# Performance work log

Measured on AMD Instinct MI355X. Metric: run time of the kernel, lower is better.

The kernel has to match this reference:

```python
import jax, jax.numpy as jnp
import numpy as np

INPUT_DIM = 128
D_MODEL = 128
BATCH = 8192
EPS = 1e-5  # torch LayerNorm default


def setup_inputs() -> dict:
    key = jax.random.key(0)
    k1, k2, k3 = jax.random.split(key, 3)
    x = jax.random.normal(k1, (BATCH, INPUT_DIM), dtype=jnp.float32)
    # Per-feature Linear(1, d_model): weight is a d_model vector per feature.
    W = jax.random.normal(k2, (INPUT_DIM, D_MODEL), dtype=jnp.float32) * (1.0 / np.sqrt(D_MODEL))
    b = jax.random.normal(k3, (INPUT_DIM, D_MODEL), dtype=jnp.float32) * 0.02
    gamma = jnp.ones((D_MODEL,), dtype=jnp.float32)
    beta = jnp.zeros((D_MODEL,), dtype=jnp.float32)
    return {"x": x, "W": W, "b": b, "gamma": gamma, "beta": beta}


def reference(x, W, b, gamma, beta):
    # Fused equivalent of the per-feature Linear loop + stack(dim=0):
    # out[f, n, d] = x[n, f] * W[f, d] + b[f, d]  -> [input_dim, batch, d_model]
    emb = x.T[:, :, None] * W[:, None, :] + b[:, None, :]
    # LayerNorm over last dim (d_model), eps=1e-5, elementwise affine.
    mean = jnp.mean(emb, axis=-1, keepdims=True)
    var = jnp.mean(jnp.square(emb - mean), axis=-1, keepdims=True)
    normed = (emb - mean) * jax.lax.rsqrt(var + EPS)
    out = normed * gamma + beta
    # Dropout is identity in eval mode.
    return out
```

## Files before the change

kernel.cpp:

```cpp
#include <hip/hip_runtime.h>

#define F_DIM   128
#define D_DIM   128
#define BATCH_N 8192
#define LN_EPS  1e-5f
#define ROWS_PER_BLOCK 64

__global__ __launch_bounds__(256) void fused_emb_ln_kernel(const float* __restrict__ x,
                                                           const float* __restrict__ W,
                                                           const float* __restrict__ b,
                                                           const float* __restrict__ gamma,
                                                           const float* __restrict__ beta,
                                                           float* __restrict__ out) {
    const int tid   = threadIdx.x;
    const int f     = blockIdx.x >> 7;
    const int nbase = (blockIdx.x & 127) * ROWS_PER_BLOCK;

    __shared__ float r1[128], r2[128], r3[128];
    __shared__ float sWg[128], sBg[128], sBe[128];

    float w = 0.f, bb = 0.f, g = 0.f, be = 0.f;
    if (tid < 128) {
        w  = W[f * D_DIM + tid];
        bb = b[f * D_DIM + tid];
        g  = gamma[tid];
        be = beta[tid];
        r1[tid] = w; r2[tid] = bb;
    }
    __syncthreads();
    for (int off = 64; off > 0; off >>= 1) {
        if (tid < off) { r1[tid] += r1[tid + off]; r2[tid] += r2[tid + off]; }
        __syncthreads();
    }
    const float inv = 1.0f / 128.0f;
    const float mw  = r1[0] * inv;
    const float mbm = r2[0] * inv;
    __syncthreads();
    if (tid < 128) {
        const float wc = w - mw;
        const float bc = bb - mbm;
        r1[tid] = wc * wc; r2[tid] = wc * bc; r3[tid] = bc * bc;
        sWg[tid] = wc * g; sBg[tid] = bc * g; sBe[tid] = be;
    }
    __syncthreads();
    for (int off = 64; off > 0; off >>= 1) {
        if (tid < off) { r1[tid] += r1[tid + off]; r2[tid] += r2[tid + off]; r3[tid] += r3[tid + off]; }
        __syncthreads();
    }
    const float A  = r1[0] * inv;
    const float B2 = 2.0f * r2[0] * inv;
    const float Cp = r3[0] * inv + LN_EPS;

    const int dv = tid & 31;
    const int r0 = tid >> 5;
    const float4* Wg4 = (const float4*)sWg;
    const float4* Bg4 = (const float4*)sBg;
    const float4* Be4 = (const float4*)sBe;
    const float4 w0 = Wg4[dv];
    const float4 b0 = Bg4[dv];
    const float4 e0 = Be4[dv];

    float4* out4 = (float4*)out;
    #pragma unroll
    for (int it = 0; it < ROWS_PER_BLOCK / 8; ++it) {
        const int n  = nbase + it * 8 + r0;
        const float xf = x[n * F_DIM + f];

        float var = fmaf(xf, fmaf(xf, A, B2), Cp);
        var = fmaxf(var, 1e-7f);
        const float rsq = rsqrtf(var);
        const float xr  = xf * rsq;

        float4 o;
        o.x = fmaf(xr, w0.x, fmaf(rsq, b0.x, e0.x));
        o.y = fmaf(xr, w0.y, fmaf(rsq, b0.y, e0.y));
        o.z = fmaf(xr, w0.z, fmaf(rsq, b0.z, e0.z));
        o.w = fmaf(xr, w0.w, fmaf(rsq, b0.w, e0.w));

        out4[(f * BATCH_N + n) * 32 + dv] = o;
    }
}

extern "C" void kernel_launch(void* const* d_in, const int* in_sizes, int n_in,
                              void* d_out, int out_size, void* d_ws, size_t ws_size,
                              hipStream_t stream) {
    const float* x     = (const float*)d_in[0];
    const float* W     = (const float*)d_in[1];
    const float* b     = (const float*)d_in[2];
    const float* gamma = (const float*)d_in[3];
    const float* beta  = (const float*)d_in[4];
    float* out = (float*)d_out;
    (void)d_ws; (void)ws_size;

    const int nblocks = F_DIM * (BATCH_N / ROWS_PER_BLOCK);
    fused_emb_ln_kernel<<<dim3(nblocks), dim3(256), 0, stream>>>(x, W, b, gamma, beta, out);
}
```

Measured before the change: 541.9 us.

## Split per-feature LN stats into prep kernel, stream outputs with nontemporal stores

Moves the per-feature mean/variance statistics of W and b into a small prep kernel that uses wavefront shuffles and writes the results to workspace. The streaming kernel now reads these precomputed values, uses far fewer and larger blocks (512 rows each), and writes its output with nontemporal stores. This removes the redundant per-block shared-memory reductions and barriers and aims to ease cache pressure on the 512 MB output write. In exchange it adds a second kernel launch and a round trip through workspace.

```diff
diff --git a/kernel.cpp b/kernel.cpp
--- a/kernel.cpp
+++ b/kernel.cpp
@@ -4,80 +4,100 @@
 #define D_DIM   128
 #define BATCH_N 8192
 #define LN_EPS  1e-5f
-#define ROWS_PER_BLOCK 64
 
-__global__ __launch_bounds__(256) void fused_emb_ln_kernel(const float* __restrict__ x,
-                                                           const float* __restrict__ W,
-                                                           const float* __restrict__ b,
-                                                           const float* __restrict__ gamma,
-                                                           const float* __restrict__ beta,
-                                                           float* __restrict__ out) {
-    const int tid   = threadIdx.x;
-    const int f     = blockIdx.x >> 7;
-    const int nbase = (blockIdx.x & 127) * ROWS_PER_BLOCK;
+#define CHUNKS          16
+#define ROWS_PER_BLOCK  (BATCH_N / CHUNKS)
+#define ITERS           (ROWS_PER_BLOCK / 8)
 
-    __shared__ float r1[128], r2[128], r3[128];
-    __shared__ float sWg[128], sBg[128], sBe[128];
+typedef float fx4 __attribute__((ext_vector_type(4)));
 
-    float w = 0.f, bb = 0.f, g = 0.f, be = 0.f;
-    if (tid < 128) {
-        w  = W[f * D_DIM + tid];
-        bb = b[f * D_DIM + tid];
-        g  = gamma[tid];
-        be = beta[tid];
-        r1[tid] = w; r2[tid] = bb;
-    }
-    __syncthreads();
-    for (int off = 64; off > 0; off >>= 1) {
-        if (tid < off) { r1[tid] += r1[tid + off]; r2[tid] += r2[tid + off]; }
-        __syncthreads();
+
+__global__ __launch_bounds__(64) void prep_kernel(const float* __restrict__ W,
+                                                  const float* __restrict__ b,
+                                                  const float* __restrict__ gamma,
+                                                  float* __restrict__ ws) {
+    const int f = blockIdx.x;
+    const int t = threadIdx.x;
+
+    const float2 w2 = ((const float2*)W)[f * 64 + t];
+    const float2 b2 = ((const float2*)b)[f * 64 + t];
+    const float2 g2 = ((const float2*)gamma)[t];
+
+    float sw = w2.x + w2.y;
+    float sb = b2.x + b2.y;
+    #pragma unroll
+    for (int off = 32; off > 0; off >>= 1) {
+        sw += __shfl_xor(sw, off);
+        sb += __shfl_xor(sb, off);
     }
     const float inv = 1.0f / 128.0f;
-    const float mw  = r1[0] * inv;
-    const float mbm = r2[0] * inv;
-    __syncthreads();
-    if (tid < 128) {
-        const float wc = w - mw;
-        const float bc = bb - mbm;
-        r1[tid] = wc * wc; r2[tid] = wc * bc; r3[tid] = bc * bc;
-        sWg[tid] = wc * g; sBg[tid] = bc * g; sBe[tid] = be;
+    const float mw = sw * inv;
+    const float mb = sb * inv;
+
+    const float wcx = w2.x - mw, wcy = w2.y - mw;
+    const float bcx = b2.x - mb, bcy = b2.y - mb;
+
+    float a  = wcx * wcx + wcy * wcy;
+    float bm = wcx * bcx + wcy * bcy;
+    float c  = bcx * bcx + bcy * bcy;
+    #pragma unroll
+    for (int off = 32; off > 0; off >>= 1) {
+        a  += __shfl_xor(a, off);
+        bm += __shfl_xor(bm, off);
+        c  += __shfl_xor(c, off);
     }
-    __syncthreads();
-    for (int off = 64; off > 0; off >>= 1) {
-        if (tid < off) { r1[tid] += r1[tid + off]; r2[tid] += r2[tid + off]; r3[tid] += r3[tid + off]; }
-        __syncthreads();
+
+    float* P = ws;
+    float* Q = ws + 128 * 128;
+    float* S = ws + 2 * 128 * 128;
+    ((float2*)P)[f * 64 + t] = make_float2(wcx * g2.x, wcy * g2.y);
+    ((float2*)Q)[f * 64 + t] = make_float2(bcx * g2.x, bcy * g2.y);
+    if (t == 0) {
+        S[f * 4 + 0] = a * inv;
+        S[f * 4 + 1] = 2.0f * bm * inv;
+        S[f * 4 + 2] = c * inv + LN_EPS;
     }
-    const float A  = r1[0] * inv;
-    const float B2 = 2.0f * r2[0] * inv;
-    const float Cp = r3[0] * inv + LN_EPS;
+}
 
-    const int dv = tid & 31;
-    const int r0 = tid >> 5;
-    const float4* Wg4 = (const float4*)sWg;
-    const float4* Bg4 = (const float4*)sBg;
-    const float4* Be4 = (const float4*)sBe;
-    const float4 w0 = Wg4[dv];
-    const float4 b0 = Bg4[dv];
-    const float4 e0 = Be4[dv];
+__global__ __launch_bounds__(256) void stream_kernel(const float* __restrict__ x,
+                                                     const float* __restrict__ beta,
+                                                     const float* __restrict__ ws,
+                                                     float* __restrict__ out) {
+    const int f     = blockIdx.x >> 4;
+    const int nbase = (blockIdx.x & (CHUNKS - 1)) * ROWS_PER_BLOCK;
+    const int dv    = threadIdx.x & 31;
+    const int r0    = threadIdx.x >> 5;
 
-    float4* out4 = (float4*)out;
-    #pragma unroll
-    for (int it = 0; it < ROWS_PER_BLOCK / 8; ++it) {
-        const int n  = nbase + it * 8 + r0;
-        const float xf = x[n * F_DIM + f];
+    const float4* P4 = (const float4*)ws + f * 32;
+    const float4* Q4 = (const float4*)(ws + 128 * 128) + f * 32;
+    const float*  S  = ws + 2 * 128 * 128 + f * 4;
+
+    const float4 w0 = P4[dv];
+    const float4 b0 = Q4[dv];
+    const float4 e0 = ((const float4*)beta)[dv];
+    const float  A  = S[0];
+    const float  B2 = S[1];
+    const float  Cp = S[2];
+
+    const float* xp = x + (nbase + r0) * F_DIM + f;
+    fx4* op = (fx4*)out + (size_t)(f * BATCH_N + nbase + r0) * 32 + dv;
+
+    #pragma unroll 4
+    for (int it = 0; it < ITERS; ++it) {
+        const float xf = xp[it * 8 * F_DIM];
 
         float var = fmaf(xf, fmaf(xf, A, B2), Cp);
         var = fmaxf(var, 1e-7f);
         const float rsq = rsqrtf(var);
         const float xr  = xf * rsq;
 
-        float4 o;
+        fx4 o;
         o.x = fmaf(xr, w0.x, fmaf(rsq, b0.x, e0.x));
         o.y = fmaf(xr, w0.y, fmaf(rsq, b0.y, e0.y));
         o.z = fmaf(xr, w0.z, fmaf(rsq, b0.z, e0.z));
         o.w = fmaf(xr, w0.w, fmaf(rsq, b0.w, e0.w));
 
-        out4[(f * BATCH_N + n) * 32 + dv] = o;
+        __builtin_nontemporal_store(o, op + it * 8 * 32);
     }
 }
 
@@ -90,8 +110,9 @@
     const float* gamma = (const float*)d_in[3];
     const float* beta  = (const float*)d_in[4];
     float* out = (float*)d_out;
-    (void)d_ws; (void)ws_size;
+    float* ws  = (float*)d_ws;
+    (void)in_sizes; (void)n_in; (void)out_size; (void)ws_size;
 
-    const int nblocks = F_DIM * (BATCH_N / ROWS_PER_BLOCK);
-    fused_emb_ln_kernel<<<dim3(nblocks), dim3(256), 0, stream>>>(x, W, b, gamma, beta, out);
+    prep_kernel<<<dim3(F_DIM), dim3(64), 0, stream>>>(W, b, gamma, ws);
+    stream_kernel<<<dim3(F_DIM * CHUNKS), dim3(256), 0, stream>>>(x, beta, ws, out);
 }
```

New measurement: 535.9 us. About the same (-1.1%).
